# Kernel tuning notes

Hardware: AMD Instinct MI355X
Metric: run time of the kernel (lower is better)

Reference implementation:

```python
import jax, jax.numpy as jnp
import numpy as np

LN_EPS = 1e-5


def setup_inputs() -> dict:
    key = jax.random.key(0)
    ks = jax.random.split(key, 8)
    N, c_z, H, C = 256, 128, 4, 32
    s = 0.02  # small init scale for stable softmax
    return {
        "z": jax.random.normal(ks[0], (N, N, c_z), dtype=jnp.float32),
        "ln_g": jnp.ones((c_z,), jnp.float32),
        "ln_b": jnp.zeros((c_z,), jnp.float32),
        "Wb": jax.random.normal(ks[1], (c_z, H), dtype=jnp.float32) * s,
        "Wq": jax.random.normal(ks[2], (c_z, H, C), dtype=jnp.float32) * s,
        "Wk": jax.random.normal(ks[3], (c_z, H, C), dtype=jnp.float32) * s,
        "Wv": jax.random.normal(ks[4], (c_z, H, C), dtype=jnp.float32) * s,
        "Wg": jax.random.normal(ks[5], (c_z, H, C), dtype=jnp.float32) * s,
        "bg": jnp.ones((H, C), jnp.float32),
        "Wo": jax.random.normal(ks[6], (H, C, c_z), dtype=jnp.float32) * s,
        "bo": jnp.zeros((c_z,), jnp.float32),
    }


def reference(z, ln_g, ln_b, Wb, Wq, Wk, Wv, Wg, bg, Wo, bo):
    # TriangleAttention, node_type='starting_node' (Algorithm 13).
    # z: (N, N, c_z)
    C = Wq.shape[-1]
    # LayerNorm over c_z
    mu = jnp.mean(z, axis=-1, keepdims=True)
    var = jnp.var(z, axis=-1, keepdims=True)
    x = (z - mu) * jax.lax.rsqrt(var + LN_EPS) * ln_g + ln_b
    # pairwise additive bias: b[h, j, k] = (x @ Wb)[j, k, h]
    b = jnp.einsum('jkz,zh->hjk', x, Wb)
    # per-head projections; attention over second residue axis (-2),
    # first residue axis i acts as batch
    q = jnp.einsum('ijz,zhc->ijhc', x, Wq)
    k = jnp.einsum('ijz,zhc->ijhc', x, Wk)
    v = jnp.einsum('ijz,zhc->ijhc', x, Wv)
    scores = jnp.einsum('iqhc,ikhc->hiqk', q, k) / jnp.sqrt(jnp.asarray(C, x.dtype))
    scores = scores + b[:, None, :, :]  # broadcast bias over batch axis i
    a = jax.nn.softmax(scores, axis=-1)  # (h, i, q, k)
    o = jnp.einsum('hiqk,ikhc->iqhc', a, v)
    g = jax.nn.sigmoid(jnp.einsum('ijz,zhc->ijhc', x, Wg) + bg)
    o = o * g
    out = jnp.einsum('iqhc,hcz->iqz', o, Wo) + bo
    return out
```

## Files before the change

### kernel.cpp

```cpp
#include <hip/hip_runtime.h>
#include <hip/hip_bf16.h>
#include <math.h>


#define NN 256
#define CZ 128

typedef __attribute__((ext_vector_type(8))) short bf16x8;
typedef __attribute__((ext_vector_type(4))) float f32x4;

__device__ __forceinline__ f32x4 mfma16(bf16x8 a, bf16x8 b, f32x4 c) {
  return __builtin_amdgcn_mfma_f32_16x16x32_bf16(a, b, c, 0, 0, 0);
}
__device__ __forceinline__ unsigned short f2bf(float f) {
  unsigned b = __float_as_uint(f);
  return (unsigned short)((b + 0x7FFFu + ((b >> 16) & 1u)) >> 16);
}

__global__ __launch_bounds__(128) void k_prep(const float* __restrict__ Wq, const float* __restrict__ Wk,
                                              const float* __restrict__ Wv, const float* __restrict__ Wg,
                                              const float* __restrict__ Wo, unsigned short* __restrict__ Wt) {
  int n = blockIdx.x, t = threadIdx.x;
  const float* srcs[5] = {Wq, Wk, Wv, Wg, Wo};
  float v = srcs[n >> 7][t * 128 + (n & 127)];
  Wt[n * 128 + t] = f2bf(v);
}

__global__ __launch_bounds__(256) void k_ln(const float* __restrict__ z,
                                            const float* __restrict__ ln_g,
                                            const float* __restrict__ ln_b,
                                            const float* __restrict__ Wb,
                                            unsigned short* __restrict__ xb,
                                            float* __restrict__ bT) {
  int wave = threadIdx.x >> 6, lane = threadIdx.x & 63;
  int pos = blockIdx.x * 4 + wave;
  float2 v = ((const float2*)(z + (size_t)pos * CZ))[lane];
  float s = v.x + v.y, sq = v.x * v.x + v.y * v.y;
#pragma unroll
  for (int o = 1; o < 64; o <<= 1) { s += __shfl_xor(s, o); sq += __shfl_xor(sq, o); }
  float mean = s * (1.0f / CZ);
  float var = sq * (1.0f / CZ) - mean * mean;
  float rstd = rsqrtf(var + 1e-5f);
  int c0 = lane * 2;
  float x0 = (v.x - mean) * rstd * ln_g[c0] + ln_b[c0];
  float x1 = (v.y - mean) * rstd * ln_g[c0 + 1] + ln_b[c0 + 1];
  unsigned pk = (unsigned)f2bf(x0) | ((unsigned)f2bf(x1) << 16);
  ((unsigned*)(xb + (size_t)pos * CZ))[lane] = pk;
  float4 w0 = *(const float4*)(Wb + c0 * 4);
  float4 w1 = *(const float4*)(Wb + (c0 + 1) * 4);
  float b0 = x0 * w0.x + x1 * w1.x;
  float b1 = x0 * w0.y + x1 * w1.y;
  float b2 = x0 * w0.z + x1 * w1.z;
  float b3 = x0 * w0.w + x1 * w1.w;
#pragma unroll
  for (int o = 1; o < 64; o <<= 1) {
    b0 += __shfl_xor(b0, o); b1 += __shfl_xor(b1, o);
    b2 += __shfl_xor(b2, o); b3 += __shfl_xor(b3, o);
  }
  if (lane == 0) {
    int j = pos >> 8, kk = pos & 255;
    bT[0 * 65536 + kk * 256 + j] = b0;
    bT[1 * 65536 + kk * 256 + j] = b1;
    bT[2 * 65536 + kk * 256 + j] = b2;
    bT[3 * 65536 + kk * 256 + j] = b3;
  }
}

__global__ __launch_bounds__(256, 3) void k_head(const unsigned short* __restrict__ xb,
                                                 const unsigned short* __restrict__ Wt,
                                                 const float* __restrict__ bT,
                                                 const float* __restrict__ bg,
                                                 unsigned short* __restrict__ og) {
  __shared__ unsigned short ks[256][40];
  __shared__ unsigned short vt[32][264];
  __shared__ unsigned short qs[4][32][40];
  int i = blockIdx.x, h = blockIdx.y;
  int t = threadIdx.x, w = t >> 6, lane = t & 63, l16 = lane & 15, g = lane >> 4;
  const float sc = 0.17677669529663687f;

  bf16x8 qa[2][2];
  f32x4 gt[2][2][2];

#pragma unroll
  for (int rh = 0; rh < 2; rh++) {
    int r0 = w * 64 + rh * 32;
    bf16x8 xa[2][4];
#pragma unroll
    for (int m = 0; m < 2; m++)
#pragma unroll
      for (int kt = 0; kt < 4; kt++)
        xa[m][kt] = *(const bf16x8*)(xb + (size_t)(i * 256 + r0 + m * 16 + l16) * CZ + kt * 32 + g * 8);
    f32x4 d[2][2];
#pragma unroll
    for (int m = 0; m < 2; m++)
#pragma unroll
      for (int n = 0; n < 2; n++) d[m][n] = (f32x4){0.f, 0.f, 0.f, 0.f};
#pragma unroll
    for (int kt = 0; kt < 4; kt++)
#pragma unroll
      for (int n = 0; n < 2; n++) {
        bf16x8 b = *(const bf16x8*)(Wt + (size_t)(128 + h * 32 + n * 16 + l16) * CZ + kt * 32 + g * 8);
#pragma unroll
        for (int m = 0; m < 2; m++) d[m][n] = mfma16(xa[m][kt], b, d[m][n]);
      }
#pragma unroll
    for (int m = 0; m < 2; m++)
#pragma unroll
      for (int n = 0; n < 2; n++)
#pragma unroll
        for (int r = 0; r < 4; r++) ks[r0 + m * 16 + g * 4 + r][n * 16 + l16] = f2bf(d[m][n][r]);
#pragma unroll
    for (int m = 0; m < 2; m++)
#pragma unroll
      for (int n = 0; n < 2; n++) d[m][n] = (f32x4){0.f, 0.f, 0.f, 0.f};
#pragma unroll
    for (int kt = 0; kt < 4; kt++)
#pragma unroll
      for (int n = 0; n < 2; n++) {
        bf16x8 b = *(const bf16x8*)(Wt + (size_t)(256 + h * 32 + n * 16 + l16) * CZ + kt * 32 + g * 8);
#pragma unroll
        for (int m = 0; m < 2; m++) d[m][n] = mfma16(xa[m][kt], b, d[m][n]);
      }
#pragma unroll
    for (int m = 0; m < 2; m++)
#pragma unroll
      for (int n = 0; n < 2; n++) {
        ushort4 pk;
        pk.x = f2bf(d[m][n][0]); pk.y = f2bf(d[m][n][1]);
        pk.z = f2bf(d[m][n][2]); pk.w = f2bf(d[m][n][3]);
        *(ushort4*)&vt[n * 16 + l16][r0 + m * 16 + g * 4] = pk;
      }
#pragma unroll
    for (int m = 0; m < 2; m++)
#pragma unroll
      for (int n = 0; n < 2; n++) d[m][n] = (f32x4){0.f, 0.f, 0.f, 0.f};
#pragma unroll
    for (int kt = 0; kt < 4; kt++)
#pragma unroll
      for (int n = 0; n < 2; n++) {
        bf16x8 b = *(const bf16x8*)(Wt + (size_t)(0 + h * 32 + n * 16 + l16) * CZ + kt * 32 + g * 8);
#pragma unroll
        for (int m = 0; m < 2; m++) d[m][n] = mfma16(xa[m][kt], b, d[m][n]);
      }
#pragma unroll
    for (int m = 0; m < 2; m++)
#pragma unroll
      for (int n = 0; n < 2; n++)
#pragma unroll
        for (int r = 0; r < 4; r++) qs[w][m * 16 + g * 4 + r][n * 16 + l16] = f2bf(d[m][n][r]);
#pragma unroll
    for (int m = 0; m < 2; m++) qa[rh][m] = *(const bf16x8*)&qs[w][m * 16 + l16][g * 8];
#pragma unroll
    for (int m = 0; m < 2; m++)
#pragma unroll
      for (int n = 0; n < 2; n++) d[m][n] = (f32x4){0.f, 0.f, 0.f, 0.f};
#pragma unroll
    for (int kt = 0; kt < 4; kt++)
#pragma unroll
      for (int n = 0; n < 2; n++) {
        bf16x8 b = *(const bf16x8*)(Wt + (size_t)(384 + h * 32 + n * 16 + l16) * CZ + kt * 32 + g * 8);
#pragma unroll
        for (int m = 0; m < 2; m++) d[m][n] = mfma16(xa[m][kt], b, d[m][n]);
      }
    float bgv0 = bg[h * 32 + l16], bgv1 = bg[h * 32 + 16 + l16];
#pragma unroll
    for (int m = 0; m < 2; m++)
#pragma unroll
      for (int n = 0; n < 2; n++)
#pragma unroll
        for (int r = 0; r < 4; r++)
          gt[rh][m][n][r] = 1.0f / (1.0f + __expf(-(d[m][n][r] + (n ? bgv1 : bgv0))));
  }
  __syncthreads();

  const float* bb = bT + (size_t)h * 65536;
#pragma unroll
  for (int qh = 0; qh < 2; qh++) {
    int rq = w * 64 + qh * 32;
    f32x4 oat[2][2], lsum[2];
#pragma unroll
    for (int m = 0; m < 2; m++) {
      lsum[m] = (f32x4){0.f, 0.f, 0.f, 0.f};
#pragma unroll
      for (int n = 0; n < 2; n++) oat[m][n] = (f32x4){0.f, 0.f, 0.f, 0.f};
    }
    for (int kc = 0; kc < 8; kc++) {
      bf16x8 kb[2];
#pragma unroll
      for (int n = 0; n < 2; n++) kb[n] = *(const bf16x8*)&ks[kc * 32 + n * 16 + l16][g * 8];
      f32x4 p[2][2];
#pragma unroll
      for (int m = 0; m < 2; m++)
#pragma unroll
        for (int n = 0; n < 2; n++) {
          f32x4 s = mfma16(qa[qh][m], kb[n], (f32x4){0.f, 0.f, 0.f, 0.f});
          float4 bv = *(const float4*)(bb + (size_t)(kc * 32 + n * 16 + l16) * 256 + rq + m * 16 + g * 4);
          p[m][n][0] = __expf(s[0] * sc + bv.x);
          p[m][n][1] = __expf(s[1] * sc + bv.y);
          p[m][n][2] = __expf(s[2] * sc + bv.z);
          p[m][n][3] = __expf(s[3] * sc + bv.w);
          lsum[m] += p[m][n];
        }
#pragma unroll
      for (int m = 0; m < 2; m++)
#pragma unroll
        for (int n = 0; n < 2; n++)
#pragma unroll
          for (int r = 0; r < 4; r++) qs[w][m * 16 + g * 4 + r][n * 16 + l16] = f2bf(p[m][n][r]);
      bf16x8 pa[2], vb[2];
#pragma unroll
      for (int m = 0; m < 2; m++) pa[m] = *(const bf16x8*)&qs[w][m * 16 + l16][g * 8];
#pragma unroll
      for (int n = 0; n < 2; n++) vb[n] = *(const bf16x8*)&vt[n * 16 + l16][kc * 32 + g * 8];
#pragma unroll
      for (int m = 0; m < 2; m++)
#pragma unroll
        for (int n = 0; n < 2; n++) oat[m][n] = mfma16(pa[m], vb[n], oat[m][n]);
    }
#pragma unroll
    for (int m = 0; m < 2; m++)
#pragma unroll
      for (int off = 1; off < 16; off <<= 1)
#pragma unroll
        for (int r = 0; r < 4; r++) lsum[m][r] += __shfl_xor(lsum[m][r], off);
#pragma unroll
    for (int m = 0; m < 2; m++) {
      f32x4 inv;
#pragma unroll
      for (int r = 0; r < 4; r++) inv[r] = 1.0f / lsum[m][r];
#pragma unroll
      for (int n = 0; n < 2; n++)
#pragma unroll
        for (int r = 0; r < 4; r++)
          qs[w][m * 16 + g * 4 + r][n * 16 + l16] = f2bf(oat[m][n][r] * inv[r] * gt[qh][m][n][r]);
    }
#pragma unroll
    for (int e = 0; e < 4; e++) {
      int idx = e * 64 + lane;
      int row = idx >> 3, c4 = (idx & 7) * 4;
      *(ushort4*)(og + (size_t)(i * 256 + rq + row) * 128 + h * 32 + c4) = *(ushort4*)&qs[w][row][c4];
    }
  }
}

__global__ __launch_bounds__(256) void k_out(const unsigned short* __restrict__ og,
                                             const unsigned short* __restrict__ WoT,
                                             const float* __restrict__ bo,
                                             float* __restrict__ out) {
  int t = threadIdx.x, w = t >> 6, lane = t & 63, l16 = lane & 15, g = lane >> 4;
  int wr = w >> 1, wc = w & 1;
  int pbase = blockIdx.x * 128 + wr * 64;
  int cbase = wc * 64;
  f32x4 acc[4][4];
#pragma unroll
  for (int m = 0; m < 4; m++)
#pragma unroll
    for (int n = 0; n < 4; n++) acc[m][n] = (f32x4){0.f, 0.f, 0.f, 0.f};
#pragma unroll
  for (int kt = 0; kt < 4; kt++) {
    bf16x8 a[4], b[4];
#pragma unroll
    for (int m = 0; m < 4; m++)
      a[m] = *(const bf16x8*)(og + (size_t)(pbase + m * 16 + l16) * 128 + kt * 32 + g * 8);
#pragma unroll
    for (int n = 0; n < 4; n++)
      b[n] = *(const bf16x8*)(WoT + (size_t)(cbase + n * 16 + l16) * 128 + kt * 32 + g * 8);
#pragma unroll
    for (int m = 0; m < 4; m++)
#pragma unroll
      for (int n = 0; n < 4; n++) acc[m][n] = mfma16(a[m], b[n], acc[m][n]);
  }
#pragma unroll
  for (int n = 0; n < 4; n++) {
    int zc = cbase + n * 16 + l16;
    float bv = bo[zc];
#pragma unroll
    for (int m = 0; m < 4; m++) {
#pragma unroll
      for (int r = 0; r < 4; r++)
        out[(size_t)(pbase + m * 16 + g * 4 + r) * 128 + zc] = acc[m][n][r] + bv;
    }
  }
}

extern "C" void kernel_launch(void* const* d_in, const int* in_sizes, int n_in,
                              void* d_out, int out_size, void* d_ws, size_t ws_size,
                              hipStream_t stream) {
  const float* z    = (const float*)d_in[0];
  const float* ln_g = (const float*)d_in[1];
  const float* ln_b = (const float*)d_in[2];
  const float* Wb   = (const float*)d_in[3];
  const float* Wq   = (const float*)d_in[4];
  const float* Wk   = (const float*)d_in[5];
  const float* Wv   = (const float*)d_in[6];
  const float* Wg   = (const float*)d_in[7];
  const float* bg   = (const float*)d_in[8];
  const float* Wo   = (const float*)d_in[9];
  const float* bo   = (const float*)d_in[10];
  float* out = (float*)d_out;

  char* ws = (char*)d_ws;
  unsigned short* xb = (unsigned short*)(ws + 0);
  float*          bT = (float*)(ws + 16777216);
  unsigned short* Wt = (unsigned short*)(ws + 17825792);
  unsigned short* og = (unsigned short*)(ws + 17989632);

  k_prep<<<640, 128, 0, stream>>>(Wq, Wk, Wv, Wg, Wo, Wt);
  k_ln<<<16384, 256, 0, stream>>>(z, ln_g, ln_b, Wb, xb, bT);
  k_head<<<dim3(256, 4), 256, 0, stream>>>(xb, Wt, bT, bg, og);
  k_out<<<512, 256, 0, stream>>>(og, Wt + 512 * 128, bo, out);
}
```

Baseline: 223.2 us.

## Compute transposed attention fragments in registers, removing LDS round-trips for Q and P

The attention kernel now computes S^T (K times Q) with the bias loaded straight into the MFMA accumulator. Q and P fragments are moved between lanes with shuffles instead of being staged through per-wave shared memory, and the exponent uses exp2 with log2(e) folded into the bias and Q scale. The bias is stored in natural row order, the sigmoid gate is kept packed as bf16 to save registers, and occupancy is raised to 4 blocks per SM. This targets LDS traffic and sync latency in the inner softmax loop, at the cost of more shuffles and lower gate precision.

```diff
diff --git a/kernel.cpp b/kernel.cpp
--- a/kernel.cpp
+++ b/kernel.cpp
@@ -16,14 +16,35 @@
   unsigned b = __float_as_uint(f);
   return (unsigned short)((b + 0x7FFFu + ((b >> 16) & 1u)) >> 16);
 }
+__device__ __forceinline__ float bf2f(unsigned short u) { return __uint_as_float((unsigned)u << 16); }
+__device__ __forceinline__ unsigned packbf(float a, float b) {
+  return (unsigned)f2bf(a) | ((unsigned)f2bf(b) << 16);
+}
+__device__ __forceinline__ bf16x8 remap_frag(unsigned pk00, unsigned pk01,
+                                             unsigned pk10, unsigned pk11,
+                                             int srcA, int srcB, bool hi) {
+  unsigned a0 = (unsigned)__shfl((int)pk00, srcA);
+  unsigned b0 = (unsigned)__shfl((int)pk10, srcA);
+  unsigned a1 = (unsigned)__shfl((int)pk01, srcA);
+  unsigned b1 = (unsigned)__shfl((int)pk11, srcA);
+  unsigned a2 = (unsigned)__shfl((int)pk00, srcB);
+  unsigned b2 = (unsigned)__shfl((int)pk10, srcB);
+  unsigned a3 = (unsigned)__shfl((int)pk01, srcB);
+  unsigned b3 = (unsigned)__shfl((int)pk11, srcB);
+  uint4 u;
+  u.x = hi ? b0 : a0;
+  u.y = hi ? b1 : a1;
+  u.z = hi ? b2 : a2;
+  u.w = hi ? b3 : a3;
+  return *(bf16x8*)&u;
+}
 
 __global__ __launch_bounds__(128) void k_prep(const float* __restrict__ Wq, const float* __restrict__ Wk,
                                               const float* __restrict__ Wv, const float* __restrict__ Wg,
                                               const float* __restrict__ Wo, unsigned short* __restrict__ Wt) {
-  int n = blockIdx.x, t = threadIdx.x;
-  const float* srcs[5] = {Wq, Wk, Wv, Wg, Wo};
-  float v = srcs[n >> 7][t * 128 + (n & 127)];
-  Wt[n * 128 + t] = f2bf(v);
+  int sec = blockIdx.y, n = blockIdx.x, t = threadIdx.x;
+  const float* s = sec == 0 ? Wq : sec == 1 ? Wk : sec == 2 ? Wv : sec == 3 ? Wg : Wo;
+  Wt[(sec * 128 + n) * 128 + t] = f2bf(s[t * 128 + n]);
 }
 
 __global__ __launch_bounds__(256) void k_ln(const float* __restrict__ z,
@@ -31,7 +52,7 @@
                                             const float* __restrict__ ln_b,
                                             const float* __restrict__ Wb,
                                             unsigned short* __restrict__ xb,
-                                            float* __restrict__ bT) {
+                                            float* __restrict__ bN) {
   int wave = threadIdx.x >> 6, lane = threadIdx.x & 63;
   int pos = blockIdx.x * 4 + wave;
   float2 v = ((const float2*)(z + (size_t)pos * CZ))[lane];
@@ -58,28 +79,31 @@
     b2 += __shfl_xor(b2, o); b3 += __shfl_xor(b3, o);
   }
   if (lane == 0) {
+    const float L2E = 1.4426950408889634f;
     int j = pos >> 8, kk = pos & 255;
-    bT[0 * 65536 + kk * 256 + j] = b0;
-    bT[1 * 65536 + kk * 256 + j] = b1;
-    bT[2 * 65536 + kk * 256 + j] = b2;
-    bT[3 * 65536 + kk * 256 + j] = b3;
-  }
-}
-
-__global__ __launch_bounds__(256, 3) void k_head(const unsigned short* __restrict__ xb,
+    bN[0 * 65536 + j * 256 + kk] = b0 * L2E;
+    bN[1 * 65536 + j * 256 + kk] = b1 * L2E;
+    bN[2 * 65536 + j * 256 + kk] = b2 * L2E;
+    bN[3 * 65536 + j * 256 + kk] = b3 * L2E;
+  }
+}
+
+__global__ __launch_bounds__(256, 4) void k_head(const unsigned short* __restrict__ xb,
                                                  const unsigned short* __restrict__ Wt,
-                                                 const float* __restrict__ bT,
+                                                 const float* __restrict__ bN,
                                                  const float* __restrict__ bg,
                                                  unsigned short* __restrict__ og) {
   __shared__ unsigned short ks[256][40];
   __shared__ unsigned short vt[32][264];
-  __shared__ unsigned short qs[4][32][40];
   int i = blockIdx.x, h = blockIdx.y;
   int t = threadIdx.x, w = t >> 6, lane = t & 63, l16 = lane & 15, g = lane >> 4;
-  const float sc = 0.17677669529663687f;
-
-  bf16x8 qa[2][2];
-  f32x4 gt[2][2][2];
+  const int srcA = l16 + 32 * (g & 1);
+  const int srcB = srcA + 16;
+  const bool hi = g >= 2;
+  const float sc2 = 0.25503486f;
+
+  bf16x8 qa[4];
+  unsigned gtp[4][2][2];
 
 #pragma unroll
   for (int rh = 0; rh < 2; rh++) {
@@ -90,155 +114,176 @@
 #pragma unroll
       for (int kt = 0; kt < 4; kt++)
         xa[m][kt] = *(const bf16x8*)(xb + (size_t)(i * 256 + r0 + m * 16 + l16) * CZ + kt * 32 + g * 8);
-    f32x4 d[2][2];
-#pragma unroll
-    for (int m = 0; m < 2; m++)
-#pragma unroll
-      for (int n = 0; n < 2; n++) d[m][n] = (f32x4){0.f, 0.f, 0.f, 0.f};
-#pragma unroll
-    for (int kt = 0; kt < 4; kt++)
+
+    {
+      bf16x8 wf[2][4];
+#pragma unroll
+      for (int n = 0; n < 2; n++)
+#pragma unroll
+        for (int kt = 0; kt < 4; kt++)
+          wf[n][kt] = *(const bf16x8*)(Wt + (size_t)(128 + h * 32 + n * 16 + l16) * CZ + kt * 32 + g * 8);
+      f32x4 d[2][2];
+#pragma unroll
+      for (int m = 0; m < 2; m++)
+#pragma unroll
+        for (int n = 0; n < 2; n++) d[m][n] = (f32x4){0.f, 0.f, 0.f, 0.f};
+#pragma unroll
+      for (int kt = 0; kt < 4; kt++)
+#pragma unroll
+        for (int m = 0; m < 2; m++)
+#pragma unroll
+          for (int n = 0; n < 2; n++) d[m][n] = mfma16(wf[n][kt], xa[m][kt], d[m][n]);
+#pragma unroll
+      for (int m = 0; m < 2; m++)
+#pragma unroll
+        for (int n = 0; n < 2; n++) {
+          ushort4 pk4;
+          pk4.x = f2bf(d[m][n][0]); pk4.y = f2bf(d[m][n][1]);
+          pk4.z = f2bf(d[m][n][2]); pk4.w = f2bf(d[m][n][3]);
+          *(ushort4*)&ks[r0 + m * 16 + l16][n * 16 + g * 4] = pk4;
+        }
+    }
+    {
+      bf16x8 wf[2][4];
+#pragma unroll
+      for (int n = 0; n < 2; n++)
+#pragma unroll
+        for (int kt = 0; kt < 4; kt++)
+          wf[n][kt] = *(const bf16x8*)(Wt + (size_t)(256 + h * 32 + n * 16 + l16) * CZ + kt * 32 + g * 8);
+      f32x4 d[2][2];
+#pragma unroll
+      for (int m = 0; m < 2; m++)
+#pragma unroll
+        for (int n = 0; n < 2; n++) d[m][n] = (f32x4){0.f, 0.f, 0.f, 0.f};
+#pragma unroll
+      for (int kt = 0; kt < 4; kt++)
+#pragma unroll
+        for (int m = 0; m < 2; m++)
+#pragma unroll
+          for (int n = 0; n < 2; n++) d[m][n] = mfma16(xa[m][kt], wf[n][kt], d[m][n]);
+#pragma unroll
+      for (int m = 0; m < 2; m++)
+#pragma unroll
+        for (int n = 0; n < 2; n++) {
+          ushort4 pk4;
+          pk4.x = f2bf(d[m][n][0]); pk4.y = f2bf(d[m][n][1]);
+          pk4.z = f2bf(d[m][n][2]); pk4.w = f2bf(d[m][n][3]);
+          *(ushort4*)&vt[n * 16 + l16][r0 + m * 16 + g * 4] = pk4;
+        }
+    }
+    {
+      bf16x8 wf[2][4];
+#pragma unroll
+      for (int n = 0; n < 2; n++)
+#pragma unroll
+        for (int kt = 0; kt < 4; kt++)
+          wf[n][kt] = *(const bf16x8*)(Wt + (size_t)(0 + h * 32 + n * 16 + l16) * CZ + kt * 32 + g * 8);
+      f32x4 d[2][2];
+#pragma unroll
+      for (int m = 0; m < 2; m++)
+#pragma unroll
+        for (int n = 0; n < 2; n++) d[m][n] = (f32x4){0.f, 0.f, 0.f, 0.f};
+#pragma unroll
+      for (int kt = 0; kt < 4; kt++)
+#pragma unroll
+        for (int m = 0; m < 2; m++)
+#pragma unroll
+          for (int n = 0; n < 2; n++) d[m][n] = mfma16(wf[n][kt], xa[m][kt], d[m][n]);
+#pragma unroll
+      for (int m = 0; m < 2; m++) {
+        unsigned pk00 = packbf(d[m][0][0] * sc2, d[m][0][1] * sc2);
+        unsigned pk01 = packbf(d[m][0][2] * sc2, d[m][0][3] * sc2);
+        unsigned pk10 = packbf(d[m][1][0] * sc2, d[m][1][1] * sc2);
+        unsigned pk11 = packbf(d[m][1][2] * sc2, d[m][1][3] * sc2);
+        qa[rh * 2 + m] = remap_frag(pk00, pk01, pk10, pk11, srcA, srcB, hi);
+      }
+    }
+    {
+      bf16x8 wf[2][4];
+#pragma unroll
+      for (int n = 0; n < 2; n++)
+#pragma unroll
+        for (int kt = 0; kt < 4; kt++)
+          wf[n][kt] = *(const bf16x8*)(Wt + (size_t)(384 + h * 32 + n * 16 + l16) * CZ + kt * 32 + g * 8);
+      f32x4 d[2][2];
+#pragma unroll
+      for (int m = 0; m < 2; m++)
+#pragma unroll
+        for (int n = 0; n < 2; n++) d[m][n] = (f32x4){0.f, 0.f, 0.f, 0.f};
+#pragma unroll
+      for (int kt = 0; kt < 4; kt++)
+#pragma unroll
+        for (int m = 0; m < 2; m++)
+#pragma unroll
+          for (int n = 0; n < 2; n++) d[m][n] = mfma16(wf[n][kt], xa[m][kt], d[m][n]);
 #pragma unroll
       for (int n = 0; n < 2; n++) {
-        bf16x8 b = *(const bf16x8*)(Wt + (size_t)(128 + h * 32 + n * 16 + l16) * CZ + kt * 32 + g * 8);
-#pragma unroll
-        for (int m = 0; m < 2; m++) d[m][n] = mfma16(xa[m][kt], b, d[m][n]);
+        float4 bgv = *(const float4*)(bg + h * 32 + n * 16 + g * 4);
+#pragma unroll
+        for (int m = 0; m < 2; m++) {
+          float s0 = 1.0f / (1.0f + __expf(-(d[m][n][0] + bgv.x)));
+          float s1 = 1.0f / (1.0f + __expf(-(d[m][n][1] + bgv.y)));
+          float s2 = 1.0f / (1.0f + __expf(-(d[m][n][2] + bgv.z)));
+          float s3 = 1.0f / (1.0f + __expf(-(d[m][n][3] + bgv.w)));
+          gtp[rh * 2 + m][n][0] = packbf(s0, s1);
+          gtp[rh * 2 + m][n][1] = packbf(s2, s3);
+        }
       }
-#pragma unroll
-    for (int m = 0; m < 2; m++)
-#pragma unroll
-      for (int n = 0; n < 2; n++)
-#pragma unroll
-        for (int r = 0; r < 4; r++) ks[r0 + m * 16 + g * 4 + r][n * 16 + l16] = f2bf(d[m][n][r]);
-#pragma unroll
-    for (int m = 0; m < 2; m++)
-#pragma unroll
-      for (int n = 0; n < 2; n++) d[m][n] = (f32x4){0.f, 0.f, 0.f, 0.f};
-#pragma unroll
-    for (int kt = 0; kt < 4; kt++)
-#pragma unroll
-      for (int n = 0; n < 2; n++) {
-        bf16x8 b = *(const bf16x8*)(Wt + (size_t)(256 + h * 32 + n * 16 + l16) * CZ + kt * 32 + g * 8);
-#pragma unroll
-        for (int m = 0; m < 2; m++) d[m][n] = mfma16(xa[m][kt], b, d[m][n]);
-      }
-#pragma unroll
-    for (int m = 0; m < 2; m++)
-#pragma unroll
-      for (int n = 0; n < 2; n++) {
-        ushort4 pk;
-        pk.x = f2bf(d[m][n][0]); pk.y = f2bf(d[m][n][1]);
-        pk.z = f2bf(d[m][n][2]); pk.w = f2bf(d[m][n][3]);
-        *(ushort4*)&vt[n * 16 + l16][r0 + m * 16 + g * 4] = pk;
-      }
-#pragma unroll
-    for (int m = 0; m < 2; m++)
-#pragma unroll
-      for (int n = 0; n < 2; n++) d[m][n] = (f32x4){0.f, 0.f, 0.f, 0.f};
-#pragma unroll
-    for (int kt = 0; kt < 4; kt++)
-#pragma unroll
-      for (int n = 0; n < 2; n++) {
-        bf16x8 b = *(const bf16x8*)(Wt + (size_t)(0 + h * 32 + n * 16 + l16) * CZ + kt * 32 + g * 8);
-#pragma unroll
-        for (int m = 0; m < 2; m++) d[m][n] = mfma16(xa[m][kt], b, d[m][n]);
-      }
-#pragma unroll
-    for (int m = 0; m < 2; m++)
-#pragma unroll
-      for (int n = 0; n < 2; n++)
-#pragma unroll
-        for (int r = 0; r < 4; r++) qs[w][m * 16 + g * 4 + r][n * 16 + l16] = f2bf(d[m][n][r]);
-#pragma unroll
-    for (int m = 0; m < 2; m++) qa[rh][m] = *(const bf16x8*)&qs[w][m * 16 + l16][g * 8];
-#pragma unroll
-    for (int m = 0; m < 2; m++)
-#pragma unroll
-      for (int n = 0; n < 2; n++) d[m][n] = (f32x4){0.f, 0.f, 0.f, 0.f};
-#pragma unroll
-    for (int kt = 0; kt < 4; kt++)
-#pragma unroll
-      for (int n = 0; n < 2; n++) {
-        bf16x8 b = *(const bf16x8*)(Wt + (size_t)(384 + h * 32 + n * 16 + l16) * CZ + kt * 32 + g * 8);
-#pragma unroll
-        for (int m = 0; m < 2; m++) d[m][n] = mfma16(xa[m][kt], b, d[m][n]);
-      }
-    float bgv0 = bg[h * 32 + l16], bgv1 = bg[h * 32 + 16 + l16];
-#pragma unroll
-    for (int m = 0; m < 2; m++)
-#pragma unroll
-      for (int n = 0; n < 2; n++)
-#pragma unroll
-        for (int r = 0; r < 4; r++)
-          gt[rh][m][n][r] = 1.0f / (1.0f + __expf(-(d[m][n][r] + (n ? bgv1 : bgv0))));
+    }
   }
   __syncthreads();
 
-  const float* bb = bT + (size_t)h * 65536;
-#pragma unroll
-  for (int qh = 0; qh < 2; qh++) {
-    int rq = w * 64 + qh * 32;
-    f32x4 oat[2][2], lsum[2];
-#pragma unroll
-    for (int m = 0; m < 2; m++) {
-      lsum[m] = (f32x4){0.f, 0.f, 0.f, 0.f};
-#pragma unroll
-      for (int n = 0; n < 2; n++) oat[m][n] = (f32x4){0.f, 0.f, 0.f, 0.f};
-    }
-    for (int kc = 0; kc < 8; kc++) {
-      bf16x8 kb[2];
-#pragma unroll
-      for (int n = 0; n < 2; n++) kb[n] = *(const bf16x8*)&ks[kc * 32 + n * 16 + l16][g * 8];
-      f32x4 p[2][2];
-#pragma unroll
-      for (int m = 0; m < 2; m++)
-#pragma unroll
-        for (int n = 0; n < 2; n++) {
-          f32x4 s = mfma16(qa[qh][m], kb[n], (f32x4){0.f, 0.f, 0.f, 0.f});
-          float4 bv = *(const float4*)(bb + (size_t)(kc * 32 + n * 16 + l16) * 256 + rq + m * 16 + g * 4);
-          p[m][n][0] = __expf(s[0] * sc + bv.x);
-          p[m][n][1] = __expf(s[1] * sc + bv.y);
-          p[m][n][2] = __expf(s[2] * sc + bv.z);
-          p[m][n][3] = __expf(s[3] * sc + bv.w);
-          lsum[m] += p[m][n];
-        }
-#pragma unroll
-      for (int m = 0; m < 2; m++)
-#pragma unroll
-        for (int n = 0; n < 2; n++)
-#pragma unroll
-          for (int r = 0; r < 4; r++) qs[w][m * 16 + g * 4 + r][n * 16 + l16] = f2bf(p[m][n][r]);
-      bf16x8 pa[2], vb[2];
-#pragma unroll
-      for (int m = 0; m < 2; m++) pa[m] = *(const bf16x8*)&qs[w][m * 16 + l16][g * 8];
-#pragma unroll
-      for (int n = 0; n < 2; n++) vb[n] = *(const bf16x8*)&vt[n * 16 + l16][kc * 32 + g * 8];
-#pragma unroll
-      for (int m = 0; m < 2; m++)
-#pragma unroll
-        for (int n = 0; n < 2; n++) oat[m][n] = mfma16(pa[m], vb[n], oat[m][n]);
-    }
-#pragma unroll
-    for (int m = 0; m < 2; m++)
-#pragma unroll
-      for (int off = 1; off < 16; off <<= 1)
-#pragma unroll
-        for (int r = 0; r < 4; r++) lsum[m][r] += __shfl_xor(lsum[m][r], off);
-#pragma unroll
-    for (int m = 0; m < 2; m++) {
-      f32x4 inv;
-#pragma unroll
-      for (int r = 0; r < 4; r++) inv[r] = 1.0f / lsum[m][r];
-#pragma unroll
-      for (int n = 0; n < 2; n++)
-#pragma unroll
-        for (int r = 0; r < 4; r++)
-          qs[w][m * 16 + g * 4 + r][n * 16 + l16] = f2bf(oat[m][n][r] * inv[r] * gt[qh][m][n][r]);
-    }
-#pragma unroll
-    for (int e = 0; e < 4; e++) {
-      int idx = e * 64 + lane;
-      int row = idx >> 3, c4 = (idx & 7) * 4;
-      *(ushort4*)(og + (size_t)(i * 256 + rq + row) * 128 + h * 32 + c4) = *(ushort4*)&qs[w][row][c4];
+  f32x4 oacc[4][2];
+  float lsum[4];
+#pragma unroll
+  for (int qB = 0; qB < 4; qB++) {
+    lsum[qB] = 0.f;
+    oacc[qB][0] = (f32x4){0.f, 0.f, 0.f, 0.f};
+    oacc[qB][1] = (f32x4){0.f, 0.f, 0.f, 0.f};
+  }
+  const float* bb = bN + (size_t)h * 65536;
+#pragma unroll 2
+  for (int kc = 0; kc < 8; kc++) {
+    bf16x8 kb[2], vb[2];
+#pragma unroll
+    for (int n = 0; n < 2; n++) kb[n] = *(const bf16x8*)&ks[kc * 32 + n * 16 + l16][g * 8];
+#pragma unroll
+    for (int n = 0; n < 2; n++) vb[n] = *(const bf16x8*)&vt[n * 16 + l16][kc * 32 + g * 8];
+#pragma unroll
+    for (int qB = 0; qB < 4; qB++) {
+      int qrow = w * 64 + qB * 16 + l16;
+      float4 c0 = *(const float4*)(bb + (size_t)qrow * 256 + kc * 32 + 0 * 16 + g * 4);
+      float4 c1 = *(const float4*)(bb + (size_t)qrow * 256 + kc * 32 + 1 * 16 + g * 4);
+      f32x4 s0 = mfma16(kb[0], qa[qB], (f32x4){c0.x, c0.y, c0.z, c0.w});
+      f32x4 s1 = mfma16(kb[1], qa[qB], (f32x4){c1.x, c1.y, c1.z, c1.w});
+      float p0 = exp2f(s0[0]), p1 = exp2f(s0[1]), p2 = exp2f(s0[2]), p3 = exp2f(s0[3]);
+      float p4 = exp2f(s1[0]), p5 = exp2f(s1[1]), p6 = exp2f(s1[2]), p7 = exp2f(s1[3]);
+      lsum[qB] += ((p0 + p1) + (p2 + p3)) + ((p4 + p5) + (p6 + p7));
+      unsigned pk00 = packbf(p0, p1), pk01 = packbf(p2, p3);
+      unsigned pk10 = packbf(p4, p5), pk11 = packbf(p6, p7);
+      bf16x8 pf = remap_frag(pk00, pk01, pk10, pk11, srcA, srcB, hi);
+      oacc[qB][0] = mfma16(vb[0], pf, oacc[qB][0]);
+      oacc[qB][1] = mfma16(vb[1], pf, oacc[qB][1]);
+    }
+  }
+#pragma unroll
+  for (int qB = 0; qB < 4; qB++) {
+    float l = lsum[qB];
+    l += __shfl_xor(l, 16);
+    l += __shfl_xor(l, 32);
+    float inv = 1.0f / l;
+#pragma unroll
+    for (int nc = 0; nc < 2; nc++) {
+      float g0 = bf2f((unsigned short)(gtp[qB][nc][0] & 0xffffu));
+      float g1 = bf2f((unsigned short)(gtp[qB][nc][0] >> 16));
+      float g2 = bf2f((unsigned short)(gtp[qB][nc][1] & 0xffffu));
+      float g3 = bf2f((unsigned short)(gtp[qB][nc][1] >> 16));
+      ushort4 pk4;
+      pk4.x = f2bf(oacc[qB][nc][0] * inv * g0);
+      pk4.y = f2bf(oacc[qB][nc][1] * inv * g1);
+      pk4.z = f2bf(oacc[qB][nc][2] * inv * g2);
+      pk4.w = f2bf(oacc[qB][nc][3] * inv * g3);
+      *(ushort4*)(og + (size_t)(i * 256 + w * 64 + qB * 16 + l16) * 128 + h * 32 + nc * 16 + g * 4) = pk4;
     }
   }
 }
@@ -301,12 +346,12 @@
 
   char* ws = (char*)d_ws;
   unsigned short* xb = (unsigned short*)(ws + 0);
-  float*          bT = (float*)(ws + 16777216);
+  float*          bN = (float*)(ws + 16777216);
   unsigned short* Wt = (unsigned short*)(ws + 17825792);
   unsigned short* og = (unsigned short*)(ws + 17989632);
 
-  k_prep<<<640, 128, 0, stream>>>(Wq, Wk, Wv, Wg, Wo, Wt);
-  k_ln<<<16384, 256, 0, stream>>>(z, ln_g, ln_b, Wb, xb, bT);
-  k_head<<<dim3(256, 4), 256, 0, stream>>>(xb, Wt, bT, bg, og);
+  k_prep<<<dim3(128, 5), 128, 0, stream>>>(Wq, Wk, Wv, Wg, Wo, Wt);
+  k_ln<<<16384, 256, 0, stream>>>(z, ln_g, ln_b, Wb, xb, bN);
+  k_head<<<dim3(256, 4), 256, 0, stream>>>(xb, Wt, bN, bg, og);
   k_out<<<512, 256, 0, stream>>>(og, Wt + 512 * 128, bo, out);
 }
```

Result: faster. 213.9 us (-4.2%).
